# Optimization experiments

Measured on AMD Instinct MI355X. Metric: run time of the kernel, lower is better.

## Reference

```python
import jax, jax.numpy as jnp
import numpy as np

N = 50000

def _norm_coeffs(edge_index, n):
    # add self-loops, compute symmetric GCN normalization D^-1/2 (A+I) D^-1/2
    loops = jnp.arange(n, dtype=edge_index.dtype)
    src = jnp.concatenate([edge_index[0], loops])
    dst = jnp.concatenate([edge_index[1], loops])
    deg = jax.ops.segment_sum(jnp.ones_like(dst, dtype=jnp.float32), dst, num_segments=n)
    dinv = jnp.where(deg > 0, jax.lax.rsqrt(deg), 0.0)
    norm = dinv[src] * dinv[dst]  # [E+N]
    return src, dst, norm

def _gcn(x, W, b, src, dst, norm, n):
    h = x @ W                                   # [N, out]
    m = h[src] * norm[:, None]                  # [E+N, out] gather + scale
    return jax.ops.segment_sum(m, dst, num_segments=n) + b

def setup_inputs() -> dict:
    key = jax.random.key(0)
    ks = jax.random.split(key, 8)
    d, h = 96, 96
    E = 800000
    return {
        "x": jax.random.normal(ks[0], (N, d), jnp.float32),
        "edge_index": jax.random.randint(ks[1], (2, E), 0, N, dtype=jnp.int64),
        "h_prev": jax.random.normal(ks[2], (N, h), jnp.float32),
        "Wx": jax.random.normal(ks[3], (d, h), jnp.float32) * (1.0 / np.sqrt(d)),
        "bx": jnp.zeros((h,), jnp.float32),
        "Wuh": jax.random.normal(ks[4], (2 * h, h), jnp.float32) * (1.0 / np.sqrt(2 * h)),
        "buh": jnp.zeros((h,), jnp.float32),
        "Wch": jax.random.normal(ks[5], (2 * h, h), jnp.float32) * (1.0 / np.sqrt(2 * h)),
        "bch": jnp.zeros((h,), jnp.float32),
    }

def reference(x, edge_index, h_prev, Wx, bx, Wuh, buh, Wch, bch):
    n = x.shape[0]
    src, dst, norm = _norm_coeffs(edge_index, n)
    x_gcn = _gcn(x, Wx, bx, src, dst, norm, n)
    combined = jnp.concatenate([x_gcn, h_prev], axis=1)
    # original computes gcn_uh(combined) twice for u and r; identical math -> compute once
    g = jax.nn.sigmoid(_gcn(combined, Wuh, buh, src, dst, norm, n))
    u = g
    r = g
    combined_r = jnp.concatenate([x_gcn, r * h_prev], axis=1)
    c = jnp.tanh(_gcn(combined_r, Wch, bch, src, dst, norm, n))
    return u * h_prev + (1.0 - u) * c
```

## Files before the change

### kernel.cpp

```cpp
#include <hip/hip_runtime.h>
#include <hip/hip_bf16.h>

#define D 96
#define CAP 64
typedef long long i64;
typedef unsigned short u16;

typedef __bf16 bf16x8 __attribute__((ext_vector_type(8)));
typedef float f32x16 __attribute__((ext_vector_type(16)));

__device__ __forceinline__ float bf2f(u16 u) {
  union { unsigned u; float f; } x; x.u = ((unsigned)u) << 16; return x.f;
}
__device__ __forceinline__ void unpack8(uint4 p, float* a) {
  a[0] = bf2f((u16)(p.x & 0xffff)); a[1] = bf2f((u16)(p.x >> 16));
  a[2] = bf2f((u16)(p.y & 0xffff)); a[3] = bf2f((u16)(p.y >> 16));
  a[4] = bf2f((u16)(p.z & 0xffff)); a[5] = bf2f((u16)(p.z >> 16));
  a[6] = bf2f((u16)(p.w & 0xffff)); a[7] = bf2f((u16)(p.w >> 16));
}

__device__ __forceinline__ void split8(const float* v8, bf16x8& hi, bf16x8& lo) {
  unsigned hu[4], lu[4];
#pragma unroll
  for (int p = 0; p < 4; p++) {
    float v0 = v8[2 * p], v1 = v8[2 * p + 1];
    unsigned u0 = __float_as_uint(v0), u1 = __float_as_uint(v1);
    hu[p] = (u0 >> 16) | (u1 & 0xffff0000u);
    float l0 = v0 - __uint_as_float(u0 & 0xffff0000u);
    float l1 = v1 - __uint_as_float(u1 & 0xffff0000u);
    lu[p] = (__float_as_uint(l0) >> 16) | (__float_as_uint(l1) & 0xffff0000u);
  }
  union { uint4 q; bf16x8 v; } H, L;
  H.q = make_uint4(hu[0], hu[1], hu[2], hu[3]);
  L.q = make_uint4(lu[0], lu[1], lu[2], lu[3]);
  hi = H.v; lo = L.v;
}

__global__ __launch_bounds__(256) void k_detect(const unsigned* __restrict__ w,
                                                int* flag, int E) {
  if (threadIdx.x < 64) {
    int lane = threadIdx.x;
    int lim = (E < 2048) ? E : 2048;
    unsigned acc = 0;
    for (int j = lane; j < lim; j += 64) acc |= w[2 * j + 1];
#pragma unroll
    for (int off = 32; off > 0; off >>= 1) acc |= __shfl_down(acc, off, 64);
    if (lane == 0) *flag = (acc == 0) ? 1 : 0;
  }
}

__global__ __launch_bounds__(256) void k_wprep(const float* __restrict__ Wx,
                                               const float* __restrict__ Wuh,
                                               const float* __restrict__ Wch,
                                               u16* __restrict__ wxh, u16* __restrict__ wxl,
                                               u16* __restrict__ wuhh, u16* __restrict__ wuhl,
                                               u16* __restrict__ wchh, u16* __restrict__ wchl) {
  int cid = blockIdx.x * 256 + threadIdx.x;
  const float* W; u16 *oh, *ol; int loc;
  if (cid < 1152) { W = Wx; oh = wxh; ol = wxl; loc = cid; }
  else if (cid < 3456) { W = Wuh; oh = wuhh; ol = wuhl; loc = cid - 1152; }
  else if (cid < 5760) { W = Wch; oh = wchh; ol = wchl; loc = cid - 3456; }
  else return;
  int oct = loc / 96;
  int j = loc - oct * 96;
  int k0 = oct * 8;
  unsigned hu[4], lu[4];
#pragma unroll
  for (int p = 0; p < 4; p++) {
    float v0 = W[(size_t)(k0 + 2 * p) * D + j];
    float v1 = W[(size_t)(k0 + 2 * p + 1) * D + j];
    unsigned u0 = __float_as_uint(v0), u1 = __float_as_uint(v1);
    hu[p] = (u0 >> 16) | (u1 & 0xffff0000u);
    float l0 = v0 - __uint_as_float(u0 & 0xffff0000u);
    float l1 = v1 - __uint_as_float(u1 & 0xffff0000u);
    lu[p] = (__float_as_uint(l0) >> 16) | (__float_as_uint(l1) & 0xffff0000u);
  }
  *(uint4*)&oh[(size_t)loc * 8] = make_uint4(hu[0], hu[1], hu[2], hu[3]);
  *(uint4*)&ol[(size_t)loc * 8] = make_uint4(lu[0], lu[1], lu[2], lu[3]);
}

__global__ __launch_bounds__(256) void k_bucket(const int* __restrict__ e32,
                                                const i64* __restrict__ e64,
                                                const int* __restrict__ flagp,
                                                uint2* __restrict__ region,
                                                int* __restrict__ cntmat,
                                                int E, int N, int NB) {
  __shared__ int lofs[256];
  const int tid = threadIdx.x;
  const int blk = blockIdx.x;
  lofs[tid] = 0;
  __syncthreads();
  const int f = *flagp;
  const int chunk = (E + gridDim.x - 1) / gridDim.x;
  const int lo = blk * chunk;
  const int hi = min(E, lo + chunk);
  for (int i = lo + tid; i < hi; i += 256) {
    int d, s;
    if (f) { d = (int)e64[(size_t)E + i]; s = (int)e64[i]; }
    else   { d = e32[(size_t)E + i];      s = e32[i]; }
    if ((unsigned)d >= (unsigned)N || (unsigned)s >= (unsigned)N) continue;
    int q = d >> 8;
    int r = atomicAdd(&lofs[q], 1);
    if (r < CAP)
      region[((size_t)q * 256 + blk) * CAP + r] = make_uint2((unsigned)s, (unsigned)d);
  }
  __syncthreads();
  if (tid < NB) cntmat[blk * 256 + tid] = min(lofs[tid], CAP);
}

__global__ __launch_bounds__(256) void k_csr(const uint2* __restrict__ region,
                                             const int* __restrict__ cntmat,
                                             int* __restrict__ deg,
                                             int* __restrict__ csrp, int NB) {
  __shared__ int ldeg[256];
  __shared__ int lcsr[256 * CAP];
  const int tid = threadIdx.x;
  const int b = blockIdx.x;
  ldeg[tid] = 0;
  __syncthreads();
  int cnt = cntmat[tid * 256 + b];
  const uint2* cell = region + ((size_t)b * 256 + tid) * CAP;
  for (int k = 0; k < cnt; k++) {
    uint2 e = cell[k];
    int node = (int)(e.y & 255u);
    int r = atomicAdd(&ldeg[node], 1);
    if (r < CAP) lcsr[node * CAP + r] = (int)e.x;
  }
  __syncthreads();
  deg[(b << 8) + tid] = ldeg[tid];
  const uint4* src = (const uint4*)lcsr;
  uint4* dst = (uint4*)(csrp + ((size_t)b << 8) * CAP);
#pragma unroll
  for (int it = 0; it < (256 * CAP) / 4 / 256; it++)
    dst[tid + it * 256] = src[tid + it * 256];
}

template <int KTOT, int MODE>
__global__ __launch_bounds__(64) void gemm_mfma(
    const float* __restrict__ xin, const float* __restrict__ xg,
    const float* __restrict__ hprev, const float* __restrict__ gmul,
    const u16* __restrict__ whi, const u16* __restrict__ wlo,
    const int* __restrict__ deg, __hip_bfloat16* __restrict__ t, int N) {
  const int l = threadIdx.x;
  const int lr = l & 31;
  const int kg = l >> 5;
  const int rb = blockIdx.x * 32;
  const int row = rb + lr;
  const bool rok = row < N;

  f32x16 acc0, acc1, acc2;
#pragma unroll
  for (int i = 0; i < 16; i++) { acc0[i] = 0.f; acc1[i] = 0.f; acc2[i] = 0.f; }

#pragma unroll
  for (int s = 0; s < KTOT / 16; s++) {
    const int k0 = s * 16 + kg * 8;
    float a8[8] = {0.f, 0.f, 0.f, 0.f, 0.f, 0.f, 0.f, 0.f};
    if (rok) {
      float4 va, vb;
      if (MODE == 0) {
        const float* src = &xin[(size_t)row * D + k0];
        va = *(const float4*)src; vb = *(const float4*)(src + 4);
      } else if (16 * s < 96) {
        const float* src = &xg[(size_t)row * D + k0];
        va = *(const float4*)src; vb = *(const float4*)(src + 4);
      } else {
        const float* src = &hprev[(size_t)row * D + (k0 - 96)];
        va = *(const float4*)src; vb = *(const float4*)(src + 4);
        if (MODE == 2) {
          const float* gs = &gmul[(size_t)row * D + (k0 - 96)];
          float4 ga = *(const float4*)gs, gb = *(const float4*)(gs + 4);
          va.x *= ga.x; va.y *= ga.y; va.z *= ga.z; va.w *= ga.w;
          vb.x *= gb.x; vb.y *= gb.y; vb.z *= gb.z; vb.w *= gb.w;
        }
      }
      a8[0] = va.x; a8[1] = va.y; a8[2] = va.z; a8[3] = va.w;
      a8[4] = vb.x; a8[5] = vb.y; a8[6] = vb.z; a8[7] = vb.w;
    }
    bf16x8 ah, al;
    split8(a8, ah, al);

    const size_t wbase = ((size_t)(s * 2 + kg) * 96 + lr) * 8;
    union { uint4 q; bf16x8 v; } B0h, B1h, B2h, B0l, B1l, B2l;
    B0h.q = *(const uint4*)&whi[wbase];
    B1h.q = *(const uint4*)&whi[wbase + 32 * 8];
    B2h.q = *(const uint4*)&whi[wbase + 64 * 8];
    B0l.q = *(const uint4*)&wlo[wbase];
    B1l.q = *(const uint4*)&wlo[wbase + 32 * 8];
    B2l.q = *(const uint4*)&wlo[wbase + 64 * 8];

    acc0 = __builtin_amdgcn_mfma_f32_32x32x16_bf16(ah, B0h.v, acc0, 0, 0, 0);
    acc1 = __builtin_amdgcn_mfma_f32_32x32x16_bf16(ah, B1h.v, acc1, 0, 0, 0);
    acc2 = __builtin_amdgcn_mfma_f32_32x32x16_bf16(ah, B2h.v, acc2, 0, 0, 0);
    acc0 = __builtin_amdgcn_mfma_f32_32x32x16_bf16(al, B0h.v, acc0, 0, 0, 0);
    acc1 = __builtin_amdgcn_mfma_f32_32x32x16_bf16(al, B1h.v, acc1, 0, 0, 0);
    acc2 = __builtin_amdgcn_mfma_f32_32x32x16_bf16(al, B2h.v, acc2, 0, 0, 0);
    acc0 = __builtin_amdgcn_mfma_f32_32x32x16_bf16(ah, B0l.v, acc0, 0, 0, 0);
    acc1 = __builtin_amdgcn_mfma_f32_32x32x16_bf16(ah, B1l.v, acc1, 0, 0, 0);
    acc2 = __builtin_amdgcn_mfma_f32_32x32x16_bf16(ah, B2l.v, acc2, 0, 0, 0);
  }

  const int rbase = rb + 4 * kg;
#pragma unroll
  for (int r = 0; r < 16; r++) {
    int orow = rbase + (r & 3) + 8 * (r >> 2);
    if (orow >= N) continue;
    float dv = rsqrtf((float)deg[orow] + 1.0f);
    __hip_bfloat16* tp = &t[(size_t)orow * D];
    tp[lr]      = __float2bfloat16(acc0[r] * dv);
    tp[lr + 32] = __float2bfloat16(acc1[r] * dv);
    tp[lr + 64] = __float2bfloat16(acc2[r] * dv);
  }
}

template <int MODE>
__global__ __launch_bounds__(256) void gather_fin(
    const __hip_bfloat16* __restrict__ t, const int* __restrict__ deg,
    const int* __restrict__ csrp,
    const float* __restrict__ bias,
    const float* __restrict__ g, const float* __restrict__ hprev,
    float* __restrict__ outf, int N) {
  int idx = blockIdx.x * 256 + threadIdx.x;
  int total = N * 12;
  if (idx >= total) return;
  int v = idx / 12;
  int c8 = idx - v * 12;
  const uint4* t8 = (const uint4*)t;
  float acc[8];
  unpack8(t8[(size_t)v * 12 + c8], acc);
  int dv_i = deg[v];
  int nb = min(dv_i, CAP);
  const uint4* cp = (const uint4*)(csrp + v * CAP);
  int j = 0;
  for (; j + 8 <= nb; j += 8) {
    uint4 ia = cp[j >> 2], ib = cp[(j >> 2) + 1];
    uint4 p0 = t8[(size_t)ia.x * 12 + c8];
    uint4 p1 = t8[(size_t)ia.y * 12 + c8];
    uint4 p2 = t8[(size_t)ia.z * 12 + c8];
    uint4 p3 = t8[(size_t)ia.w * 12 + c8];
    uint4 p4 = t8[(size_t)ib.x * 12 + c8];
    uint4 p5 = t8[(size_t)ib.y * 12 + c8];
    uint4 p6 = t8[(size_t)ib.z * 12 + c8];
    uint4 p7 = t8[(size_t)ib.w * 12 + c8];
    float a0[8], a1[8], a2[8], a3[8], a4[8], a5[8], a6[8], a7[8];
    unpack8(p0, a0); unpack8(p1, a1); unpack8(p2, a2); unpack8(p3, a3);
    unpack8(p4, a4); unpack8(p5, a5); unpack8(p6, a6); unpack8(p7, a7);
#pragma unroll
    for (int q = 0; q < 8; q++)
      acc[q] += ((a0[q] + a1[q]) + (a2[q] + a3[q])) + ((a4[q] + a5[q]) + (a6[q] + a7[q]));
  }
  for (; j + 4 <= nb; j += 4) {
    uint4 ia = cp[j >> 2];
    uint4 p0 = t8[(size_t)ia.x * 12 + c8];
    uint4 p1 = t8[(size_t)ia.y * 12 + c8];
    uint4 p2 = t8[(size_t)ia.z * 12 + c8];
    uint4 p3 = t8[(size_t)ia.w * 12 + c8];
    float a0[8], a1[8], a2[8], a3[8];
    unpack8(p0, a0); unpack8(p1, a1); unpack8(p2, a2); unpack8(p3, a3);
#pragma unroll
    for (int q = 0; q < 8; q++) acc[q] += (a0[q] + a1[q]) + (a2[q] + a3[q]);
  }
  for (; j < nb; j++) {
    int s = csrp[v * CAP + j];
    float a0[8];
    unpack8(t8[(size_t)s * 12 + c8], a0);
#pragma unroll
    for (int q = 0; q < 8; q++) acc[q] += a0[q];
  }
  float dv = rsqrtf((float)dv_i + 1.0f);
  float4 bA = ((const float4*)bias)[c8 * 2];
  float4 bB = ((const float4*)bias)[c8 * 2 + 1];
  float z[8] = {dv * acc[0] + bA.x, dv * acc[1] + bA.y, dv * acc[2] + bA.z, dv * acc[3] + bA.w,
                dv * acc[4] + bB.x, dv * acc[5] + bB.y, dv * acc[6] + bB.z, dv * acc[7] + bB.w};
  float4 oA, oB;
  if (MODE == 1) {
    oA = make_float4(z[0], z[1], z[2], z[3]);
    oB = make_float4(z[4], z[5], z[6], z[7]);
  } else if (MODE == 2) {
    oA = make_float4(1.0f / (1.0f + expf(-z[0])), 1.0f / (1.0f + expf(-z[1])),
                     1.0f / (1.0f + expf(-z[2])), 1.0f / (1.0f + expf(-z[3])));
    oB = make_float4(1.0f / (1.0f + expf(-z[4])), 1.0f / (1.0f + expf(-z[5])),
                     1.0f / (1.0f + expf(-z[6])), 1.0f / (1.0f + expf(-z[7])));
  } else {
    float4 uA = ((const float4*)g)[idx * 2], uB = ((const float4*)g)[idx * 2 + 1];
    float4 hA = ((const float4*)hprev)[idx * 2], hB = ((const float4*)hprev)[idx * 2 + 1];
    oA = make_float4(uA.x * hA.x + (1.0f - uA.x) * tanhf(z[0]),
                     uA.y * hA.y + (1.0f - uA.y) * tanhf(z[1]),
                     uA.z * hA.z + (1.0f - uA.z) * tanhf(z[2]),
                     uA.w * hA.w + (1.0f - uA.w) * tanhf(z[3]));
    oB = make_float4(uB.x * hB.x + (1.0f - uB.x) * tanhf(z[4]),
                     uB.y * hB.y + (1.0f - uB.y) * tanhf(z[5]),
                     uB.z * hB.z + (1.0f - uB.z) * tanhf(z[6]),
                     uB.w * hB.w + (1.0f - uB.w) * tanhf(z[7]));
  }
  ((float4*)outf)[idx * 2] = oA;
  ((float4*)outf)[idx * 2 + 1] = oB;
}

extern "C" void kernel_launch(void* const* d_in, const int* in_sizes, int n_in,
                              void* d_out, int out_size, void* d_ws, size_t ws_size,
                              hipStream_t stream) {
  const float* x = (const float*)d_in[0];
  const int* ei32 = (const int*)d_in[1];
  const i64* ei64 = (const i64*)d_in[1];
  const unsigned* eiw = (const unsigned*)d_in[1];
  const float* hp = (const float*)d_in[2];
  const float* Wx = (const float*)d_in[3];
  const float* bx = (const float*)d_in[4];
  const float* Wuh = (const float*)d_in[5];
  const float* buh = (const float*)d_in[6];
  const float* Wch = (const float*)d_in[7];
  const float* bch = (const float*)d_in[8];
  float* out = (float*)d_out;

  const int N = in_sizes[0] / D;
  const int E = in_sizes[1] / 2;
  const size_t NF = (size_t)N * D;
  const int NB = (N + 255) >> 8;
  const int R = NB << 8;

  char* base = (char*)d_ws;
  int* flag = (int*)base;
  u16* wxh = (u16*)(base + 256);
  u16* wxl = wxh + 9216;
  u16* wuhh = wxl + 9216;
  u16* wuhl = wuhh + 18432;
  u16* wchh = wuhl + 18432;
  u16* wchl = wchh + 18432;
  int* deg = (int*)(wchl + 18432);
  int* cntmat = deg + R;
  uint2* region = (uint2*)(cntmat + 65536);
  int* csrp = (int*)(region + (size_t)NB * 256 * CAP);
  __hip_bfloat16* t = (__hip_bfloat16*)(csrp + (size_t)R * CAP);
  float* xg = (float*)((char*)t + NF * 2);
  float* g = xg + NF;

  const int gb32 = (N + 31) / 32;
  const int fb8 = (N * 12 + 255) / 256;

  k_detect<<<1, 256, 0, stream>>>(eiw, flag, E);
  k_wprep<<<23, 256, 0, stream>>>(Wx, Wuh, Wch, wxh, wxl, wuhh, wuhl, wchh, wchl);
  k_bucket<<<256, 256, 0, stream>>>(ei32, ei64, flag, region, cntmat, E, N, NB);
  k_csr<<<NB, 256, 0, stream>>>(region, cntmat, deg, csrp, NB);

  gemm_mfma<96, 0><<<gb32, 64, 0, stream>>>(x, nullptr, nullptr, nullptr, wxh, wxl, deg, t, N);
  gather_fin<1><<<fb8, 256, 0, stream>>>(t, deg, csrp, bx, nullptr, nullptr, xg, N);

  gemm_mfma<192, 1><<<gb32, 64, 0, stream>>>(nullptr, xg, hp, nullptr, wuhh, wuhl, deg, t, N);
  gather_fin<2><<<fb8, 256, 0, stream>>>(t, deg, csrp, buh, nullptr, nullptr, g, N);

  gemm_mfma<192, 2><<<gb32, 64, 0, stream>>>(nullptr, xg, hp, g, wchh, wchl, deg, t, N);
  gather_fin<3><<<fb8, 256, 0, stream>>>(t, deg, csrp, bch, g, hp, out, N);
}
```

Before: 261.0 us.

## Stage CSR indices in LDS for gather and software-pipeline GEMM A loads

The gather kernel now handles 16 nodes per 192-thread block and first copies their neighbor index lists and degrees into padded shared memory. The 12 threads that work on the same node then read indices from LDS instead of each loading the same CSR row from global memory. The GEMM moves to 4 waves per block and double-buffers the A-operand loads so the next step's loads are issued before the current step's MFMAs. The GEMM loop is no longer unrolled, and the extra LDS staging and barrier add latency, so the benefit is uncertain.

```diff
diff --git a/kernel.cpp b/kernel.cpp
--- a/kernel.cpp
+++ b/kernel.cpp
@@ -136,50 +136,51 @@
 }
 
 template <int KTOT, int MODE>
-__global__ __launch_bounds__(64) void gemm_mfma(
+__global__ __launch_bounds__(256) void gemm_mfma(
     const float* __restrict__ xin, const float* __restrict__ xg,
     const float* __restrict__ hprev, const float* __restrict__ gmul,
     const u16* __restrict__ whi, const u16* __restrict__ wlo,
     const int* __restrict__ deg, __hip_bfloat16* __restrict__ t, int N) {
-  const int l = threadIdx.x;
+  const int l = threadIdx.x & 63;
+  const int wave = threadIdx.x >> 6;
   const int lr = l & 31;
   const int kg = l >> 5;
-  const int rb = blockIdx.x * 32;
+  const int rb = blockIdx.x * 128 + wave * 32;
   const int row = rb + lr;
   const bool rok = row < N;
+  constexpr int steps = KTOT / 16;
 
   f32x16 acc0, acc1, acc2;
 #pragma unroll
   for (int i = 0; i < 16; i++) { acc0[i] = 0.f; acc1[i] = 0.f; acc2[i] = 0.f; }
 
-#pragma unroll
-  for (int s = 0; s < KTOT / 16; s++) {
-    const int k0 = s * 16 + kg * 8;
-    float a8[8] = {0.f, 0.f, 0.f, 0.f, 0.f, 0.f, 0.f, 0.f};
-    if (rok) {
-      float4 va, vb;
-      if (MODE == 0) {
-        const float* src = &xin[(size_t)row * D + k0];
-        va = *(const float4*)src; vb = *(const float4*)(src + 4);
-      } else if (16 * s < 96) {
-        const float* src = &xg[(size_t)row * D + k0];
-        va = *(const float4*)src; vb = *(const float4*)(src + 4);
-      } else {
-        const float* src = &hprev[(size_t)row * D + (k0 - 96)];
-        va = *(const float4*)src; vb = *(const float4*)(src + 4);
-        if (MODE == 2) {
-          const float* gs = &gmul[(size_t)row * D + (k0 - 96)];
-          float4 ga = *(const float4*)gs, gb = *(const float4*)(gs + 4);
-          va.x *= ga.x; va.y *= ga.y; va.z *= ga.z; va.w *= ga.w;
-          vb.x *= gb.x; vb.y *= gb.y; vb.z *= gb.z; vb.w *= gb.w;
-        }
+  auto loadA = [&](int s, float4& va, float4& vb, float4& ga, float4& gb) {
+    if (!rok) return;
+    int k0 = s * 16 + kg * 8;
+    if (MODE == 0) {
+      const float* src = &xin[(size_t)row * D + k0];
+      va = *(const float4*)src; vb = *(const float4*)(src + 4);
+    } else if (s < 6) {
+      const float* src = &xg[(size_t)row * D + k0];
+      va = *(const float4*)src; vb = *(const float4*)(src + 4);
+    } else {
+      const float* src = &hprev[(size_t)row * D + (k0 - 96)];
+      va = *(const float4*)src; vb = *(const float4*)(src + 4);
+      if (MODE == 2) {
+        const float* gs = &gmul[(size_t)row * D + (k0 - 96)];
+        ga = *(const float4*)gs; gb = *(const float4*)(gs + 4);
       }
-      a8[0] = va.x; a8[1] = va.y; a8[2] = va.z; a8[3] = va.w;
-      a8[4] = vb.x; a8[5] = vb.y; a8[6] = vb.z; a8[7] = vb.w;
     }
+  };
+
+  auto computeS = [&](int s, float4 va, float4 vb, float4 ga, float4 gb) {
+    if (MODE == 2 && s >= 6) {
+      va.x *= ga.x; va.y *= ga.y; va.z *= ga.z; va.w *= ga.w;
+      vb.x *= gb.x; vb.y *= gb.y; vb.z *= gb.z; vb.w *= gb.w;
+    }
+    float a8[8] = {va.x, va.y, va.z, va.w, vb.x, vb.y, vb.z, vb.w};
     bf16x8 ah, al;
     split8(a8, ah, al);
-
     const size_t wbase = ((size_t)(s * 2 + kg) * 96 + lr) * 8;
     union { uint4 q; bf16x8 v; } B0h, B1h, B2h, B0l, B1l, B2l;
     B0h.q = *(const uint4*)&whi[wbase];
@@ -188,7 +189,6 @@
     B0l.q = *(const uint4*)&wlo[wbase];
     B1l.q = *(const uint4*)&wlo[wbase + 32 * 8];
     B2l.q = *(const uint4*)&wlo[wbase + 64 * 8];
-
     acc0 = __builtin_amdgcn_mfma_f32_32x32x16_bf16(ah, B0h.v, acc0, 0, 0, 0);
     acc1 = __builtin_amdgcn_mfma_f32_32x32x16_bf16(ah, B1h.v, acc1, 0, 0, 0);
     acc2 = __builtin_amdgcn_mfma_f32_32x32x16_bf16(ah, B2h.v, acc2, 0, 0, 0);
@@ -198,6 +198,19 @@
     acc0 = __builtin_amdgcn_mfma_f32_32x32x16_bf16(ah, B0l.v, acc0, 0, 0, 0);
     acc1 = __builtin_amdgcn_mfma_f32_32x32x16_bf16(ah, B1l.v, acc1, 0, 0, 0);
     acc2 = __builtin_amdgcn_mfma_f32_32x32x16_bf16(ah, B2l.v, acc2, 0, 0, 0);
+  };
+
+  float4 z4 = make_float4(0.f, 0.f, 0.f, 0.f);
+  float4 va0 = z4, vb0 = z4, ga0 = z4, gb0 = z4;
+  float4 va1 = z4, vb1 = z4, ga1 = z4, gb1 = z4;
+  loadA(0, va0, vb0, ga0, gb0);
+  loadA(1, va1, vb1, ga1, gb1);
+#pragma unroll 1
+  for (int s = 0; s < steps; s += 2) {
+    computeS(s, va0, vb0, ga0, gb0);
+    if (s + 2 < steps) loadA(s + 2, va0, vb0, ga0, gb0);
+    computeS(s + 1, va1, vb1, ga1, gb1);
+    if (s + 3 < steps) loadA(s + 3, va1, vb1, ga1, gb1);
   }
 
   const int rbase = rb + 4 * kg;
@@ -214,34 +227,48 @@
 }
 
 template <int MODE>
-__global__ __launch_bounds__(256) void gather_fin(
+__global__ __launch_bounds__(192) void gather_fin(
     const __hip_bfloat16* __restrict__ t, const int* __restrict__ deg,
     const int* __restrict__ csrp,
     const float* __restrict__ bias,
     const float* __restrict__ g, const float* __restrict__ hprev,
     float* __restrict__ outf, int N) {
-  int idx = blockIdx.x * 256 + threadIdx.x;
-  int total = N * 12;
-  if (idx >= total) return;
-  int v = idx / 12;
-  int c8 = idx - v * 12;
+  __shared__ int lidx[16 * 65];
+  __shared__ int ldeg[16];
+  const int tid = threadIdx.x;
+  const int vbase = blockIdx.x * 16;
+#pragma unroll
+  for (int it = 0; it < 6; it++) {
+    int i = tid + it * 192;
+    if (i < 1024) {
+      int n = i >> 6, j = i & 63;
+      lidx[n * 65 + j] = csrp[((size_t)(vbase + n)) * CAP + j];
+    }
+  }
+  if (tid < 16) ldeg[tid] = deg[vbase + tid];
+  __syncthreads();
+  const int n = tid / 12;
+  const int c8 = tid - n * 12;
+  const int v = vbase + n;
+  if (v >= N) return;
   const uint4* t8 = (const uint4*)t;
   float acc[8];
   unpack8(t8[(size_t)v * 12 + c8], acc);
-  int dv_i = deg[v];
+  int dv_i = ldeg[n];
   int nb = min(dv_i, CAP);
-  const uint4* cp = (const uint4*)(csrp + v * CAP);
+  const int* ip = &lidx[n * 65];
   int j = 0;
   for (; j + 8 <= nb; j += 8) {
-    uint4 ia = cp[j >> 2], ib = cp[(j >> 2) + 1];
-    uint4 p0 = t8[(size_t)ia.x * 12 + c8];
-    uint4 p1 = t8[(size_t)ia.y * 12 + c8];
-    uint4 p2 = t8[(size_t)ia.z * 12 + c8];
-    uint4 p3 = t8[(size_t)ia.w * 12 + c8];
-    uint4 p4 = t8[(size_t)ib.x * 12 + c8];
-    uint4 p5 = t8[(size_t)ib.y * 12 + c8];
-    uint4 p6 = t8[(size_t)ib.z * 12 + c8];
-    uint4 p7 = t8[(size_t)ib.w * 12 + c8];
+    int s0 = ip[j],     s1 = ip[j + 1], s2 = ip[j + 2], s3 = ip[j + 3];
+    int s4 = ip[j + 4], s5 = ip[j + 5], s6 = ip[j + 6], s7 = ip[j + 7];
+    uint4 p0 = t8[(size_t)s0 * 12 + c8];
+    uint4 p1 = t8[(size_t)s1 * 12 + c8];
+    uint4 p2 = t8[(size_t)s2 * 12 + c8];
+    uint4 p3 = t8[(size_t)s3 * 12 + c8];
+    uint4 p4 = t8[(size_t)s4 * 12 + c8];
+    uint4 p5 = t8[(size_t)s5 * 12 + c8];
+    uint4 p6 = t8[(size_t)s6 * 12 + c8];
+    uint4 p7 = t8[(size_t)s7 * 12 + c8];
     float a0[8], a1[8], a2[8], a3[8], a4[8], a5[8], a6[8], a7[8];
     unpack8(p0, a0); unpack8(p1, a1); unpack8(p2, a2); unpack8(p3, a3);
     unpack8(p4, a4); unpack8(p5, a5); unpack8(p6, a6); unpack8(p7, a7);
@@ -250,18 +277,18 @@
       acc[q] += ((a0[q] + a1[q]) + (a2[q] + a3[q])) + ((a4[q] + a5[q]) + (a6[q] + a7[q]));
   }
   for (; j + 4 <= nb; j += 4) {
-    uint4 ia = cp[j >> 2];
-    uint4 p0 = t8[(size_t)ia.x * 12 + c8];
-    uint4 p1 = t8[(size_t)ia.y * 12 + c8];
-    uint4 p2 = t8[(size_t)ia.z * 12 + c8];
-    uint4 p3 = t8[(size_t)ia.w * 12 + c8];
+    int s0 = ip[j], s1 = ip[j + 1], s2 = ip[j + 2], s3 = ip[j + 3];
+    uint4 p0 = t8[(size_t)s0 * 12 + c8];
+    uint4 p1 = t8[(size_t)s1 * 12 + c8];
+    uint4 p2 = t8[(size_t)s2 * 12 + c8];
+    uint4 p3 = t8[(size_t)s3 * 12 + c8];
     float a0[8], a1[8], a2[8], a3[8];
     unpack8(p0, a0); unpack8(p1, a1); unpack8(p2, a2); unpack8(p3, a3);
 #pragma unroll
     for (int q = 0; q < 8; q++) acc[q] += (a0[q] + a1[q]) + (a2[q] + a3[q]);
   }
   for (; j < nb; j++) {
-    int s = csrp[v * CAP + j];
+    int s = ip[j];
     float a0[8];
     unpack8(t8[(size_t)s * 12 + c8], a0);
 #pragma unroll
@@ -272,6 +299,7 @@
   float4 bB = ((const float4*)bias)[c8 * 2 + 1];
   float z[8] = {dv * acc[0] + bA.x, dv * acc[1] + bA.y, dv * acc[2] + bA.z, dv * acc[3] + bA.w,
                 dv * acc[4] + bB.x, dv * acc[5] + bB.y, dv * acc[6] + bB.z, dv * acc[7] + bB.w};
+  const size_t oidx = (size_t)v * 12 + c8;
   float4 oA, oB;
   if (MODE == 1) {
     oA = make_float4(z[0], z[1], z[2], z[3]);
@@ -282,8 +310,8 @@
     oB = make_float4(1.0f / (1.0f + expf(-z[4])), 1.0f / (1.0f + expf(-z[5])),
                      1.0f / (1.0f + expf(-z[6])), 1.0f / (1.0f + expf(-z[7])));
   } else {
-    float4 uA = ((const float4*)g)[idx * 2], uB = ((const float4*)g)[idx * 2 + 1];
-    float4 hA = ((const float4*)hprev)[idx * 2], hB = ((const float4*)hprev)[idx * 2 + 1];
+    float4 uA = ((const float4*)g)[oidx * 2], uB = ((const float4*)g)[oidx * 2 + 1];
+    float4 hA = ((const float4*)hprev)[oidx * 2], hB = ((const float4*)hprev)[oidx * 2 + 1];
     oA = make_float4(uA.x * hA.x + (1.0f - uA.x) * tanhf(z[0]),
                      uA.y * hA.y + (1.0f - uA.y) * tanhf(z[1]),
                      uA.z * hA.z + (1.0f - uA.z) * tanhf(z[2]),
@@ -293,8 +321,8 @@
                      uB.z * hB.z + (1.0f - uB.z) * tanhf(z[6]),
                      uB.w * hB.w + (1.0f - uB.w) * tanhf(z[7]));
   }
-  ((float4*)outf)[idx * 2] = oA;
-  ((float4*)outf)[idx * 2 + 1] = oB;
+  ((float4*)outf)[oidx * 2] = oA;
+  ((float4*)outf)[oidx * 2 + 1] = oB;
 }
 
 extern "C" void kernel_launch(void* const* d_in, const int* in_sizes, int n_in,
@@ -335,20 +363,20 @@
   float* xg = (float*)((char*)t + NF * 2);
   float* g = xg + NF;
 
-  const int gb32 = (N + 31) / 32;
-  const int fb8 = (N * 12 + 255) / 256;
+  const int gb = (N + 127) / 128;
+  const int fb = (N + 15) / 16;
 
   k_detect<<<1, 256, 0, stream>>>(eiw, flag, E);
   k_wprep<<<23, 256, 0, stream>>>(Wx, Wuh, Wch, wxh, wxl, wuhh, wuhl, wchh, wchl);
   k_bucket<<<256, 256, 0, stream>>>(ei32, ei64, flag, region, cntmat, E, N, NB);
   k_csr<<<NB, 256, 0, stream>>>(region, cntmat, deg, csrp, NB);
 
-  gemm_mfma<96, 0><<<gb32, 64, 0, stream>>>(x, nullptr, nullptr, nullptr, wxh, wxl, deg, t, N);
-  gather_fin<1><<<fb8, 256, 0, stream>>>(t, deg, csrp, bx, nullptr, nullptr, xg, N);
-
-  gemm_mfma<192, 1><<<gb32, 64, 0, stream>>>(nullptr, xg, hp, nullptr, wuhh, wuhl, deg, t, N);
-  gather_fin<2><<<fb8, 256, 0, stream>>>(t, deg, csrp, buh, nullptr, nullptr, g, N);
-
-  gemm_mfma<192, 2><<<gb32, 64, 0, stream>>>(nullptr, xg, hp, g, wchh, wchl, deg, t, N);
-  gather_fin<3><<<fb8, 256, 0, stream>>>(t, deg, csrp, bch, g, hp, out, N);
-}
+  gemm_mfma<96, 0><<<gb, 256, 0, stream>>>(x, nullptr, nullptr, nullptr, wxh, wxl, deg, t, N);
+  gather_fin<1><<<fb, 192, 0, stream>>>(t, deg, csrp, bx, nullptr, nullptr, xg, N);
+
+  gemm_mfma<192, 1><<<gb, 256, 0, stream>>>(nullptr, xg, hp, nullptr, wuhh, wuhl, deg, t, N);
+  gather_fin<2><<<fb, 192, 0, stream>>>(t, deg, csrp, buh, nullptr, nullptr, g, N);
+
+  gemm_mfma<192, 2><<<gb, 256, 0, stream>>>(nullptr, xg, hp, g, wchh, wchl, deg, t, N);
+  gather_fin<3><<<fb, 192, 0, stream>>>(t, deg, csrp, bch, g, hp, out, N);
+}
```

New measurement: 294.5 us. 1.13x slower.
